# Optimization experiments

Hardware: AMD Instinct MI355X
Metric: run time of the kernel (lower is better)

## Reference

```python
import jax, jax.numpy as jnp
import numpy as np

SHIFT = 8  # shift_range init kwarg
EPS = 1e-12  # F.normalize default eps (x / max(||x||, eps))


def setup_inputs() -> dict:
    key = jax.random.key(0)
    k1, k2 = jax.random.split(key)
    grd_feature = jax.random.normal(k1, (64, 64, 24, 24), dtype=jnp.float32)
    sat_feature = jax.random.normal(k2, (64, 64, 64, 64), dtype=jnp.float32)
    return {"grd_feature": grd_feature, "sat_feature": sat_feature}


def reference(grd_feature, sat_feature):
    M, C, Hs, Ws = sat_feature.shape
    N, _, H, W = grd_feature.shape
    kH = min(H, Hs - 2 * SHIFT, 24)
    kW = min(W, Ws - 2 * SHIFT, 24)
    # center-crop ground features to kernel size
    grd = grd_feature[:, :, H // 2 - kH // 2: H // 2 + kH // 2,
                      W // 2 - kW // 2: W // 2 + kW // 2]  # [N,C,kH,kW]
    # crop sat features to search window (kernel + 2*shift)
    sat = sat_feature[:, :, Hs // 2 - SHIFT - kH // 2: Hs // 2 + SHIFT + kH // 2,
                      Ws // 2 - SHIFT - kW // 2: Ws // 2 + SHIFT + kW // 2]  # [M,C,Hi,Wi]
    # cross-correlation: repeat+grouped-conv in torch == plain conv2d here -> [M,N,Ho,Wo]
    corr = jax.lax.conv_general_dilated(
        sat, grd, window_strides=(1, 1), padding='VALID',
        dimension_numbers=('NCHW', 'OIHW', 'NCHW'))
    Ho, Wo = corr.shape[2], corr.shape[3]
    flat_idx = jnp.argmax(corr.reshape(M, N, Ho * Wo), axis=-1)  # [M,N]
    hy = flat_idx // Wo
    wx = flat_idx % Wo

    def gather_patch(sat_j, h, w):  # sat_j: [C,Hi,Wi]
        return jax.lax.dynamic_slice(sat_j, (0, h, w), (C, kH, kW))

    # vectorized patch gather over (M, N) -> [M,N,C,kH,kW]
    patches = jax.vmap(
        lambda sj, hs, ws: jax.vmap(lambda h, w: gather_patch(sj, h, w))(hs, ws)
    )(sat, hy, wx)

    pn = patches.reshape(M * N, -1)
    pn = pn / jnp.maximum(jnp.linalg.norm(pn, axis=-1, keepdims=True), EPS)
    pn = pn.reshape(M, N, C, kH, kW)
    gn = grd.reshape(N, -1)
    gn = gn / jnp.maximum(jnp.linalg.norm(gn, axis=-1, keepdims=True), EPS)
    gn = gn.reshape(N, C, kH, kW)
    similarity_matrix = jnp.einsum('mnchw,nchw->mn', pn, gn)
    sat_f = patches[M - 1, N - 1]  # last gathered (unnormalized) patch, as in torch
    return similarity_matrix, sat_f
```

## Files before the change

### kernel.cpp

```cpp
#include <hip/hip_runtime.h>
#include <hip/hip_bf16.h>
#include <math.h>


typedef float f32x16 __attribute__((ext_vector_type(16)));
typedef short short8 __attribute__((ext_vector_type(8)));

#define SATT_H 0u
#define GRDT_H 3276800u
#define CORR_O 4456448u
#define WIN2_O 5701632u
#define GN2_O  5720128u
#define IDX_O  5720192u
#define CEX_O  5721216u
#define S2G_O  5721600u

__global__ __launch_bounds__(256) void make_satT(const float* __restrict__ sat,
                                                 __hip_bfloat16* __restrict__ sth,
                                                 float* __restrict__ S2g) {
    __shared__ __hip_bfloat16 th[40 * 66];
    int m = blockIdx.x / 40, r = blockIdx.x % 40;
    int tid = threadIdx.x;
    const float* base = sat + (size_t)m * 262144 + (12 + r) * 64 + 12;
    for (int k = 0; k < 10; k++) {
        int idx = tid + 256 * k;
        int c = idx / 40, w2 = idx % 40;
        th[w2 * 66 + c] = __float2bfloat16(base[c * 4096 + w2]);
    }
    __syncthreads();
    __hip_bfloat16* dh = sth + (size_t)m * 102400 + r * 640;
    for (int k = 0; k < 10; k++) {
        int idx = tid + 256 * k;
        int cc = idx / 640, rem = idx - cc * 640;
        int w2 = rem >> 4, cl = rem & 15;
        dh[cc * 25600 + w2 * 16 + cl] = th[w2 * 66 + cc * 16 + cl];
    }
    if (tid < 40) {
        float s = 0.0f;
        for (int c = 0; c < 64; c++) {
            float v = __bfloat162float(th[tid * 66 + c]);
            s += v * v;
        }
        S2g[m * 1600 + r * 40 + tid] = s;
    }
}

__global__ __launch_bounds__(256) void make_grdT(const float* __restrict__ grd,
                                                 __hip_bfloat16* __restrict__ gth,
                                                 float* __restrict__ gn2) {
    __shared__ __hip_bfloat16 t[32 * 577];
    __shared__ float red[4];
    int bid = blockIdx.x;
    int n = bid >> 1, ch = bid & 1;
    int tid = threadIdx.x;
    const float* src = grd + (size_t)n * 36864 + ch * 32 * 576;
    float s = 0.0f;
    for (int k = 0; k < 72; k++) {
        int idx = tid + 256 * k;
        int cl = idx / 576, ij = idx % 576;
        float v = src[idx];
        s += v * v;
        t[cl * 577 + ij] = __float2bfloat16(v);
    }
    for (int off = 32; off; off >>= 1) s += __shfl_down(s, off);
    if ((tid & 63) == 0) red[tid >> 6] = s;
    __syncthreads();
    if (tid == 0) atomicAdd(&gn2[n], red[0] + red[1] + red[2] + red[3]);
    for (int k = 0; k < 72; k++) {
        int idx = tid + 256 * k;
        int ij = idx >> 5, cl = idx & 31;
        int c = ch * 32 + cl;
        gth[((size_t)((c >> 4) * 576 + ij)) * 1024 + n * 16 + (c & 15)] = t[cl * 577 + ij];
    }
}

__global__ __launch_bounds__(256) void make_win2(const float* __restrict__ S2g,
                                                 float* __restrict__ win2) {
    __shared__ float S2[40][41];
    __shared__ float RS[40][18];
    int m = blockIdx.x, tid = threadIdx.x;
    for (int k = 0; k < 7; k++) {
        int idx = tid + 256 * k;
        if (idx < 1600) S2[idx / 40][idx % 40] = S2g[m * 1600 + idx];
    }
    __syncthreads();
    for (int k = 0; k < 3; k++) {
        int idx = tid + 256 * k;
        if (idx < 680) {
            int r = idx / 17, x = idx % 17;
            float s = 0.0f;
            for (int j = 0; j < 24; j++) s += S2[r][x + j];
            RS[r][x] = s;
        }
    }
    __syncthreads();
    for (int k = 0; k < 2; k++) {
        int idx = tid + 256 * k;
        if (idx < 289) {
            int y = idx / 17, x = idx % 17;
            float s = 0.0f;
            for (int i2 = 0; i2 < 24; i2++) s += RS[y + i2][x];
            win2[m * 289 + idx] = s;
        }
    }
}

__global__ __launch_bounds__(384, 3) void corr_mfma(const __hip_bfloat16* __restrict__ sth,
                                                    const __hip_bfloat16* __restrict__ gth,
                                                    float* __restrict__ corr) {
    __shared__ __align__(16) __hip_bfloat16 satW[760 * 16];

    int bid = blockIdx.x;
    int xcd = bid & 7, slot = bid >> 3;
    int m = xcd * 8 + (slot >> 3), iq = slot & 7;
    int tid = threadIdx.x;
    int w = tid >> 6, l = tid & 63;
    int ln31 = l & 31, h = l >> 5;

    int rowbase[2];
#pragma unroll
    for (int t = 0; t < 2; t++) {
        int tile = (w < 4) ? (w + 4 * t) : (w + 4);
        int p = tile * 32 + ln31;
        if (p > 288) p = 288;
        rowbase[t] = (p / 17) * 40 + (p % 17);
    }
    f32x16 acc[2][2];
#pragma unroll
    for (int t = 0; t < 2; t++) {
        acc[t][0] = (f32x16)0.0f;
        acc[t][1] = (f32x16)0.0f;
    }

    const __hip_bfloat16* gbase = gth + (size_t)(iq * 72) * 1024 + ln31 * 16 + h * 8;

#define BLOADR(B0, B1, CC, IJL) {                                               \
        const __hip_bfloat16* p_ = gbase + ((size_t)(CC) * 576 + (IJL)) * 1024; \
        B0 = *(const short8*)p_;                                                \
        B1 = *(const short8*)(p_ + 512);                                        \
    }
#define COMPUTE(IJL, B0, B1) {                                                  \
        int il_ = (IJL) / 24;                                                   \
        int pixoff_ = il_ * 40 + ((IJL) - il_ * 24);                            \
        if (w < 4) {                                                            \
            _Pragma("unroll")                                                   \
            for (int t = 0; t < 2; t++) {                                       \
                int ao = (rowbase[t] + pixoff_) * 32 + h * 16;                  \
                short8 af = *(const short8*)((const char*)satW + ao);           \
                acc[t][0] = __builtin_amdgcn_mfma_f32_32x32x16_bf16(af, B0, acc[t][0], 0, 0, 0); \
                acc[t][1] = __builtin_amdgcn_mfma_f32_32x32x16_bf16(af, B1, acc[t][1], 0, 0, 0); \
            }                                                                   \
        } else {                                                                \
            int ao = (rowbase[0] + pixoff_) * 32 + h * 16;                      \
            short8 af = *(const short8*)((const char*)satW + ao);               \
            acc[0][0] = __builtin_amdgcn_mfma_f32_32x32x16_bf16(af, B0, acc[0][0], 0, 0, 0); \
            acc[0][1] = __builtin_amdgcn_mfma_f32_32x32x16_bf16(af, B1, acc[0][1], 0, 0, 0); \
        }                                                                       \
    }

#pragma unroll
    for (int cc = 0; cc < 4; cc++) {
        __syncthreads();
        const __hip_bfloat16* satb = sth + (size_t)m * 102400 + cc * 25600 + iq * 1920;
#pragma unroll
        for (int k2 = 0; k2 < 4; k2++) {
            int s = tid + 384 * k2;
            if (s < 1520) {
                float4 v = *(const float4*)(satb + s * 8);
                *(float4*)((char*)satW + s * 16) = v;
            }
        }
        short8 x0, x1, y0, y1, z0, z1;
        BLOADR(x0, x1, cc, 0);
        BLOADR(y0, y1, cc, 1);
        BLOADR(z0, z1, cc, 2);
        __syncthreads();

        for (int ijg = 0; ijg < 24; ijg++) {
            int base = ijg * 3;
            COMPUTE(base + 0, x0, x1);
            if (base + 3 < 72) BLOADR(x0, x1, cc, base + 3);
            COMPUTE(base + 1, y0, y1);
            if (base + 4 < 72) BLOADR(y0, y1, cc, base + 4);
            COMPUTE(base + 2, z0, z1);
            if (base + 5 < 72) BLOADR(z0, z1, cc, base + 5);
        }
    }

    int T = (w < 4) ? 2 : 1;
#pragma unroll
    for (int t = 0; t < 2; t++) {
        if (t >= T) break;
        int tile = (w < 4) ? (w + 4 * t) : (w + 4);
#pragma unroll
        for (int nt = 0; nt < 2; nt++)
#pragma unroll
            for (int q = 0; q < 16; q++) {
                int prow = tile * 32 + (q & 3) + 8 * (q >> 2) + 4 * h;
                if (prow < 289)
                    atomicAdd(&corr[((size_t)m * 304 + prow) * 64 + nt * 32 + ln31],
                              acc[t][nt][q]);
            }
    }
#undef BLOADR
#undef COMPUTE
}

__global__ __launch_bounds__(64) void argsim(const float* __restrict__ corr,
                                             const float* __restrict__ win2,
                                             const float* __restrict__ gn2,
                                             float* __restrict__ out,
                                             int* __restrict__ idxb) {
    int b = blockIdx.x, m = b >> 6, n = b & 63, lane = threadIdx.x;
    float bv = -3.0e38f;
    int bi = 1 << 30;
    for (int k = 0; k < 5; k++) {
        int p = lane + 64 * k;
        if (p < 289) {
            float v = corr[((size_t)m * 304 + p) * 64 + n];
            if (v > bv) { bv = v; bi = p; }
        }
    }
    for (int off = 32; off; off >>= 1) {
        float ov = __shfl_down(bv, off);
        int oi = __shfl_down(bi, off);
        if (ov > bv || (ov == bv && oi < bi)) { bv = ov; bi = oi; }
    }
    if (lane == 0) {
        float np = sqrtf(win2[m * 289 + bi]);
        float ng = sqrtf(gn2[n]);
        out[b] = bv / (fmaxf(np, 1e-12f) * fmaxf(ng, 1e-12f));
        idxb[b] = bi;
    }
}

__global__ __launch_bounds__(256) void exact63(const float* __restrict__ sat,
                                               const float* __restrict__ grd,
                                               float* __restrict__ correx) {
    int p = blockIdx.x;
    int hy = p / 17, wx = p % 17;
    int tid = threadIdx.x;
    const float* satm = sat + (size_t)63 * 262144;
    const float* grdn = grd + (size_t)63 * 36864;
    float dot = 0.0f;
    for (int e = tid; e < 36864; e += 256) {
        int c = e / 576, rem = e - c * 576;
        int i = rem / 24, j = rem - i * 24;
        dot += satm[c * 4096 + (12 + hy + i) * 64 + 12 + wx + j] * grdn[e];
    }
    for (int off = 32; off; off >>= 1) dot += __shfl_down(dot, off);
    __shared__ float red[4];
    if ((tid & 63) == 0) red[tid >> 6] = dot;
    __syncthreads();
    if (tid == 0) correx[p] = red[0] + red[1] + red[2] + red[3];
}

__global__ __launch_bounds__(256) void copy_patch(const float* __restrict__ sat,
                                                  const float* __restrict__ cex,
                                                  const float* __restrict__ win2,
                                                  const float* __restrict__ gn2,
                                                  float* __restrict__ out) {
    __shared__ float rbv[4];
    __shared__ int rbi[4];
    int tid = threadIdx.x;
    float bv = -3.0e38f;
    int bi = 1 << 30;
    for (int p = tid; p < 289; p += 256) {
        float v = cex[p];
        if (v > bv) { bv = v; bi = p; }
    }
    for (int off = 32; off; off >>= 1) {
        float ov = __shfl_down(bv, off);
        int oi = __shfl_down(bi, off);
        if (ov > bv || (ov == bv && oi < bi)) { bv = ov; bi = oi; }
    }
    if ((tid & 63) == 0) { rbv[tid >> 6] = bv; rbi[tid >> 6] = bi; }
    __syncthreads();
    if (tid == 0) {
        for (int q = 1; q < 4; q++)
            if (rbv[q] > rbv[0] || (rbv[q] == rbv[0] && rbi[q] < rbi[0])) {
                rbv[0] = rbv[q]; rbi[0] = rbi[q];
            }
        if (blockIdx.x == 0)
            out[4095] = rbv[0] / (fmaxf(sqrtf(win2[63 * 289 + rbi[0]]), 1e-12f) *
                                  fmaxf(sqrtf(gn2[63]), 1e-12f));
    }
    __syncthreads();
    int fidx = rbi[0];
    int hy = fidx / 17, wx = fidx % 17;
    int e = blockIdx.x * 256 + tid;
    int c = e / 576;
    int rem = e - c * 576;
    int rr = rem / 24, col = rem - rr * 24;
    out[4096 + e] = sat[(size_t)(63 * 64 + c) * 4096 + (12 + hy + rr) * 64 + 12 + wx + col];
}

extern "C" void kernel_launch(void* const* d_in, const int* in_sizes, int n_in,
                              void* d_out, int out_size, void* d_ws, size_t ws_size,
                              hipStream_t stream) {
    const float* grd = (const float*)d_in[0];
    const float* sat = (const float*)d_in[1];
    float* out = (float*)d_out;

    float* wsf = (float*)d_ws;
    __hip_bfloat16* sth = (__hip_bfloat16*)(wsf + SATT_H);
    __hip_bfloat16* gth = (__hip_bfloat16*)(wsf + GRDT_H);
    float* corr = wsf + CORR_O;
    float* win2 = wsf + WIN2_O;
    float* gn2  = wsf + GN2_O;
    int*   idxb = (int*)(wsf + IDX_O);
    float* cex  = wsf + CEX_O;
    float* S2g  = wsf + S2G_O;

    hipMemsetAsync(corr, 0, (size_t)1263744 * sizeof(float), stream);
    make_satT<<<2560, 256, 0, stream>>>(sat, sth, S2g);
    make_grdT<<<128, 256, 0, stream>>>(grd, gth, gn2);
    make_win2<<<64, 256, 0, stream>>>(S2g, win2);
    corr_mfma<<<512, 384, 0, stream>>>(sth, gth, corr);
    argsim<<<4096, 64, 0, stream>>>(corr, win2, gn2, out, idxb);
    exact63<<<289, 256, 0, stream>>>(sat, grd, cex);
    copy_patch<<<144, 256, 0, stream>>>(sat, cex, win2, gn2, out);
}
```

Before: 198.2 us.

## Fuse window-norm kernel into argmax and rebalance MFMA waves to four per block

Removes the separate make_win2 launch by computing the sliding-window squared-norm sums inside a per-m argsim block, which now runs 64 blocks of 256 threads instead of 4096 single-wave blocks and does the argmax with a shared-memory reduction. The corr_mfma kernel drops from 6 to 4 waves per block, so each wave handles 2 or 3 row tiles instead of 1 or 2. The win2 buffer shrinks to the single row needed by copy_patch and the memset size is reduced to match. Risks: fewer waves per block lowers latency hiding in the MFMA loop, and only 64 argsim blocks may leave much of the GPU idle.

```diff
diff --git a/kernel.cpp b/kernel.cpp
--- a/kernel.cpp
+++ b/kernel.cpp
@@ -9,11 +9,10 @@
 #define SATT_H 0u
 #define GRDT_H 3276800u
 #define CORR_O 4456448u
-#define WIN2_O 5701632u
-#define GN2_O  5720128u
-#define IDX_O  5720192u
-#define CEX_O  5721216u
-#define S2G_O  5721600u
+#define WING_O 5701632u
+#define GN2_O  5702016u
+#define CEX_O  5702080u
+#define S2G_O  5702464u
 
 __global__ __launch_bounds__(256) void make_satT(const float* __restrict__ sat,
                                                  __hip_bfloat16* __restrict__ sth,
@@ -74,38 +73,7 @@
     }
 }
 
-__global__ __launch_bounds__(256) void make_win2(const float* __restrict__ S2g,
-                                                 float* __restrict__ win2) {
-    __shared__ float S2[40][41];
-    __shared__ float RS[40][18];
-    int m = blockIdx.x, tid = threadIdx.x;
-    for (int k = 0; k < 7; k++) {
-        int idx = tid + 256 * k;
-        if (idx < 1600) S2[idx / 40][idx % 40] = S2g[m * 1600 + idx];
-    }
-    __syncthreads();
-    for (int k = 0; k < 3; k++) {
-        int idx = tid + 256 * k;
-        if (idx < 680) {
-            int r = idx / 17, x = idx % 17;
-            float s = 0.0f;
-            for (int j = 0; j < 24; j++) s += S2[r][x + j];
-            RS[r][x] = s;
-        }
-    }
-    __syncthreads();
-    for (int k = 0; k < 2; k++) {
-        int idx = tid + 256 * k;
-        if (idx < 289) {
-            int y = idx / 17, x = idx % 17;
-            float s = 0.0f;
-            for (int i2 = 0; i2 < 24; i2++) s += RS[y + i2][x];
-            win2[m * 289 + idx] = s;
-        }
-    }
-}
-
-__global__ __launch_bounds__(384, 3) void corr_mfma(const __hip_bfloat16* __restrict__ sth,
+__global__ __launch_bounds__(256, 2) void corr_mfma(const __hip_bfloat16* __restrict__ sth,
                                                     const __hip_bfloat16* __restrict__ gth,
                                                     float* __restrict__ corr) {
     __shared__ __align__(16) __hip_bfloat16 satW[760 * 16];
@@ -117,17 +85,16 @@
     int w = tid >> 6, l = tid & 63;
     int ln31 = l & 31, h = l >> 5;
 
-    int rowbase[2];
-#pragma unroll
-    for (int t = 0; t < 2; t++) {
-        int tile = (w < 4) ? (w + 4 * t) : (w + 4);
-        int p = tile * 32 + ln31;
+    int rowbase[3];
+#pragma unroll
+    for (int t = 0; t < 3; t++) {
+        int p = (w + 4 * t) * 32 + ln31;
         if (p > 288) p = 288;
         rowbase[t] = (p / 17) * 40 + (p % 17);
     }
-    f32x16 acc[2][2];
-#pragma unroll
-    for (int t = 0; t < 2; t++) {
+    f32x16 acc[3][2];
+#pragma unroll
+    for (int t = 0; t < 3; t++) {
         acc[t][0] = (f32x16)0.0f;
         acc[t][1] = (f32x16)0.0f;
     }
@@ -142,7 +109,15 @@
 #define COMPUTE(IJL, B0, B1) {                                                  \
         int il_ = (IJL) / 24;                                                   \
         int pixoff_ = il_ * 40 + ((IJL) - il_ * 24);                            \
-        if (w < 4) {                                                            \
+        if (w < 2) {                                                            \
+            _Pragma("unroll")                                                   \
+            for (int t = 0; t < 3; t++) {                                       \
+                int ao = (rowbase[t] + pixoff_) * 32 + h * 16;                  \
+                short8 af = *(const short8*)((const char*)satW + ao);           \
+                acc[t][0] = __builtin_amdgcn_mfma_f32_32x32x16_bf16(af, B0, acc[t][0], 0, 0, 0); \
+                acc[t][1] = __builtin_amdgcn_mfma_f32_32x32x16_bf16(af, B1, acc[t][1], 0, 0, 0); \
+            }                                                                   \
+        } else {                                                                \
             _Pragma("unroll")                                                   \
             for (int t = 0; t < 2; t++) {                                       \
                 int ao = (rowbase[t] + pixoff_) * 32 + h * 16;                  \
@@ -150,11 +125,6 @@
                 acc[t][0] = __builtin_amdgcn_mfma_f32_32x32x16_bf16(af, B0, acc[t][0], 0, 0, 0); \
                 acc[t][1] = __builtin_amdgcn_mfma_f32_32x32x16_bf16(af, B1, acc[t][1], 0, 0, 0); \
             }                                                                   \
-        } else {                                                                \
-            int ao = (rowbase[0] + pixoff_) * 32 + h * 16;                      \
-            short8 af = *(const short8*)((const char*)satW + ao);               \
-            acc[0][0] = __builtin_amdgcn_mfma_f32_32x32x16_bf16(af, B0, acc[0][0], 0, 0, 0); \
-            acc[0][1] = __builtin_amdgcn_mfma_f32_32x32x16_bf16(af, B1, acc[0][1], 0, 0, 0); \
         }                                                                       \
     }
 
@@ -163,8 +133,8 @@
         __syncthreads();
         const __hip_bfloat16* satb = sth + (size_t)m * 102400 + cc * 25600 + iq * 1920;
 #pragma unroll
-        for (int k2 = 0; k2 < 4; k2++) {
-            int s = tid + 384 * k2;
+        for (int k2 = 0; k2 < 6; k2++) {
+            int s = tid + 256 * k2;
             if (s < 1520) {
                 float4 v = *(const float4*)(satb + s * 8);
                 *(float4*)((char*)satW + s * 16) = v;
@@ -187,11 +157,11 @@
         }
     }
 
-    int T = (w < 4) ? 2 : 1;
-#pragma unroll
-    for (int t = 0; t < 2; t++) {
+    int T = (w < 2) ? 3 : 2;
+#pragma unroll
+    for (int t = 0; t < 3; t++) {
         if (t >= T) break;
-        int tile = (w < 4) ? (w + 4 * t) : (w + 4);
+        int tile = w + 4 * t;
 #pragma unroll
         for (int nt = 0; nt < 2; nt++)
 #pragma unroll
@@ -206,31 +176,62 @@
 #undef COMPUTE
 }
 
-__global__ __launch_bounds__(64) void argsim(const float* __restrict__ corr,
-                                             const float* __restrict__ win2,
-                                             const float* __restrict__ gn2,
-                                             float* __restrict__ out,
-                                             int* __restrict__ idxb) {
-    int b = blockIdx.x, m = b >> 6, n = b & 63, lane = threadIdx.x;
+__global__ __launch_bounds__(256) void argsim(const float* __restrict__ corr,
+                                              const float* __restrict__ S2g,
+                                              const float* __restrict__ gn2,
+                                              float* __restrict__ winG,
+                                              float* __restrict__ out) {
+    __shared__ float S2[40][41];
+    __shared__ float RS[40][18];
+    __shared__ float w2[304];
+    __shared__ float gn[64];
+    __shared__ float fbv[4][64];
+    __shared__ int   fbi[4][64];
+    int m = blockIdx.x, tid = threadIdx.x;
+    for (int k = 0; k < 7; k++) {
+        int idx = tid + 256 * k;
+        if (idx < 1600) S2[idx / 40][idx % 40] = S2g[m * 1600 + idx];
+    }
+    if (tid < 64) gn[tid] = gn2[tid];
+    __syncthreads();
+    for (int k = 0; k < 3; k++) {
+        int idx = tid + 256 * k;
+        if (idx < 680) {
+            int r = idx / 17, x = idx % 17;
+            float s = 0.0f;
+            for (int j = 0; j < 24; j++) s += S2[r][x + j];
+            RS[r][x] = s;
+        }
+    }
+    __syncthreads();
+    for (int k = 0; k < 2; k++) {
+        int idx = tid + 256 * k;
+        if (idx < 289) {
+            int y = idx / 17, x = idx % 17;
+            float s = 0.0f;
+            for (int i2 = 0; i2 < 24; i2++) s += RS[y + i2][x];
+            w2[idx] = s;
+            if (m == 63) winG[idx] = s;
+        }
+    }
+    __syncthreads();
+    int n = tid & 63, pg = tid >> 6;
     float bv = -3.0e38f;
     int bi = 1 << 30;
-    for (int k = 0; k < 5; k++) {
-        int p = lane + 64 * k;
-        if (p < 289) {
-            float v = corr[((size_t)m * 304 + p) * 64 + n];
-            if (v > bv) { bv = v; bi = p; }
-        }
-    }
-    for (int off = 32; off; off >>= 1) {
-        float ov = __shfl_down(bv, off);
-        int oi = __shfl_down(bi, off);
-        if (ov > bv || (ov == bv && oi < bi)) { bv = ov; bi = oi; }
-    }
-    if (lane == 0) {
-        float np = sqrtf(win2[m * 289 + bi]);
-        float ng = sqrtf(gn2[n]);
-        out[b] = bv / (fmaxf(np, 1e-12f) * fmaxf(ng, 1e-12f));
-        idxb[b] = bi;
+    for (int p = pg; p < 289; p += 4) {
+        float v = corr[((size_t)m * 304 + p) * 64 + n];
+        if (v > bv) { bv = v; bi = p; }
+    }
+    fbv[pg][n] = bv;
+    fbi[pg][n] = bi;
+    __syncthreads();
+    if (pg == 0) {
+        for (int q = 1; q < 4; q++) {
+            float ov = fbv[q][n];
+            int oi = fbi[q][n];
+            if (ov > bv || (ov == bv && oi < bi)) { bv = ov; bi = oi; }
+        }
+        out[m * 64 + n] = bv / (fmaxf(sqrtf(w2[bi]), 1e-12f) * fmaxf(sqrtf(gn[n]), 1e-12f));
     }
 }
 
@@ -257,7 +258,7 @@
 
 __global__ __launch_bounds__(256) void copy_patch(const float* __restrict__ sat,
                                                   const float* __restrict__ cex,
-                                                  const float* __restrict__ win2,
+                                                  const float* __restrict__ winG,
                                                   const float* __restrict__ gn2,
                                                   float* __restrict__ out) {
     __shared__ float rbv[4];
@@ -282,7 +283,7 @@
                 rbv[0] = rbv[q]; rbi[0] = rbi[q];
             }
         if (blockIdx.x == 0)
-            out[4095] = rbv[0] / (fmaxf(sqrtf(win2[63 * 289 + rbi[0]]), 1e-12f) *
+            out[4095] = rbv[0] / (fmaxf(sqrtf(winG[rbi[0]]), 1e-12f) *
                                   fmaxf(sqrtf(gn2[63]), 1e-12f));
     }
     __syncthreads();
@@ -306,18 +307,16 @@
     __hip_bfloat16* sth = (__hip_bfloat16*)(wsf + SATT_H);
     __hip_bfloat16* gth = (__hip_bfloat16*)(wsf + GRDT_H);
     float* corr = wsf + CORR_O;
-    float* win2 = wsf + WIN2_O;
+    float* winG = wsf + WING_O;
     float* gn2  = wsf + GN2_O;
-    int*   idxb = (int*)(wsf + IDX_O);
     float* cex  = wsf + CEX_O;
     float* S2g  = wsf + S2G_O;
 
-    hipMemsetAsync(corr, 0, (size_t)1263744 * sizeof(float), stream);
+    hipMemsetAsync(corr, 0, (size_t)1245632 * sizeof(float), stream);
     make_satT<<<2560, 256, 0, stream>>>(sat, sth, S2g);
     make_grdT<<<128, 256, 0, stream>>>(grd, gth, gn2);
-    make_win2<<<64, 256, 0, stream>>>(S2g, win2);
-    corr_mfma<<<512, 384, 0, stream>>>(sth, gth, corr);
-    argsim<<<4096, 64, 0, stream>>>(corr, win2, gn2, out, idxb);
+    corr_mfma<<<512, 256, 0, stream>>>(sth, gth, corr);
+    argsim<<<64, 256, 0, stream>>>(corr, S2g, gn2, winG, out);
     exact63<<<289, 256, 0, stream>>>(sat, grd, cex);
-    copy_patch<<<144, 256, 0, stream>>>(sat, cex, win2, gn2, out);
-}
+    copy_patch<<<144, 256, 0, stream>>>(sat, cex, winG, gn2, out);
+}
```

Measured after the change: 196.6 us. No clear change (-0.8%).
